# Kernel optimization log

Measured on AMD Instinct MI355X. Metric: run time of the kernel, lower is better.

Reference implementation:

```python
import jax, jax.numpy as jnp
import numpy as np
import math

DIM = 1024

def setup_inputs() -> dict:
    key = jax.random.key(0)
    ks = jax.random.split(key, 5)
    X = jax.random.normal(ks[0], (4, 2048, DIM), dtype=jnp.float32)
    # Linear params (stored as [in, out] so y = x @ W + b)
    W_in = jax.random.normal(ks[1], (DIM, 3 * DIM), dtype=jnp.float32) / math.sqrt(DIM)
    b_in = jnp.zeros((3 * DIM,), dtype=jnp.float32)
    W_out = jax.random.normal(ks[2], (DIM, DIM), dtype=jnp.float32) / math.sqrt(DIM)
    b_out = jnp.zeros((DIM,), dtype=jnp.float32)
    return {"X": X, "W_in": W_in, "b_in": b_in, "W_out": W_out, "b_out": b_out}

def reference(X, W_in, b_in, W_out, b_out):
    dim = X.shape[-1]
    QKV = X @ W_in + b_in                       # [B, S, 3*dim]
    Q, K, V = jnp.split(QKV, 3, axis=-1)        # each [B, S, dim]
    scores = jnp.einsum('bqd,bkd->bqk', Q, K) / math.sqrt(dim)  # [B, S, S]
    attn = jax.nn.softmax(scores, axis=-1)
    out = jnp.einsum('bqk,bkd->bqd', attn, V)   # [B, S, dim]
    return out @ W_out + b_out
```

## Files before the change

### kernel.cpp

```cpp
#include <hip/hip_runtime.h>
#include <hip/hip_bf16.h>
#include <math.h>

typedef __attribute__((ext_vector_type(8))) __bf16 bf16x8;
typedef __attribute__((ext_vector_type(4))) float f32x4;
typedef __attribute__((ext_vector_type(4))) unsigned int u32x4;

#define DIM 1024
#define SEQ 2048
#define BATCH 4
#define ROWS (BATCH*SEQ)

#define BAR() do { asm volatile("" ::: "memory"); __builtin_amdgcn_s_barrier(); asm volatile("" ::: "memory"); } while(0)
#define WAITV(n) asm volatile("s_waitcnt vmcnt(" #n ")" ::: "memory")
#define WAITL(n) asm volatile("s_waitcnt lgkmcnt(" #n ")" ::: "memory")
#define SCHED0() __builtin_amdgcn_sched_barrier(0)
#define PRIO(x) __builtin_amdgcn_s_setprio(x)

#define DSR(d, a, off) do { u32x4 _t; \
  asm volatile("ds_read_b128 %0, %1 offset:" #off : "=v"(_t) : "v"(a)); \
  (d) = __builtin_bit_cast(bf16x8, _t); } while(0)

__device__ __forceinline__ unsigned short f2bf(float f) {
  unsigned int u = __float_as_uint(f);
  u += 0x7FFF + ((u >> 16) & 1);
  return (unsigned short)(u >> 16);
}
__device__ __forceinline__ unsigned short to_bf_bits(float v) { return f2bf(v); }
__device__ __forceinline__ unsigned short to_bf_bits(unsigned short v) { return v; }

__device__ __forceinline__ void gload_lds16(const void* g, void* lds) {
  __builtin_amdgcn_global_load_lds((__attribute__((address_space(1))) void*)g,
                                   (__attribute__((address_space(3))) void*)lds,
                                   16, 0, 0);
}

__global__ __launch_bounds__(256)
void conv_f32_bf16(const float* __restrict__ src, unsigned short* __restrict__ dst, int n8) {
  int i = blockIdx.x * blockDim.x + threadIdx.x;
  if (i >= n8) return;
  const float4* s = reinterpret_cast<const float4*>(src) + (size_t)i * 2;
  float4 a = s[0], b = s[1];
  union { unsigned short h[8]; uint4 v; } p;
  p.h[0]=f2bf(a.x); p.h[1]=f2bf(a.y); p.h[2]=f2bf(a.z); p.h[3]=f2bf(a.w);
  p.h[4]=f2bf(b.x); p.h[5]=f2bf(b.y); p.h[6]=f2bf(b.z); p.h[7]=f2bf(b.w);
  reinterpret_cast<uint4*>(dst)[i] = p.v;
}

template<typename Tin>
__global__ __launch_bounds__(1024)
void transpose_conv(const Tin* __restrict__ src, int ldsrc, size_t sstride,
                    unsigned short* __restrict__ dst, int lddst, size_t dstride) {
  __shared__ unsigned short tile[32][33];
  const Tin* s = src + (size_t)blockIdx.z * sstride;
  unsigned short* d = dst + (size_t)blockIdx.z * dstride;
  int tx = threadIdx.x, ty = threadIdx.y;
  int r = blockIdx.y * 32 + ty, c = blockIdx.x * 32 + tx;
  tile[ty][tx] = to_bf_bits(s[(size_t)r * ldsrc + c]);
  __syncthreads();
  d[(size_t)(blockIdx.x * 32 + ty) * lddst + blockIdx.y * 32 + tx] = tile[tx][ty];
}

#define EPI_QKV 0
#define EPI_F32 1
#define EPI_BF16 2
#define EPI_BIAS_F32 3

template<int BN, int EPI>
__global__ __launch_bounds__(512, 2)
void gemm8(const unsigned short* __restrict__ A, int lda, size_t sA,
           const unsigned short* __restrict__ B, int ldb, size_t sB,
           void* __restrict__ C, int ldc, size_t sC,
           const float* __restrict__ bias, int K) {
  constexpr int NREP = BN / 64;
  constexpr int NW = 16 * NREP;
  __shared__ unsigned short As[2 * 256 * 64];
  __shared__ unsigned short Bs[2 * BN * 64];

  const int tid = threadIdx.x;
  const int lane = tid & 63, wave = tid >> 6;
  const int wm = wave >> 2, wn = wave & 3;
  const int fr = lane & 15, fk = lane >> 4;
  const int tileM = blockIdx.y * 256, tileN = blockIdx.x * BN;
  const unsigned short* Ab = A + (size_t)blockIdx.z * sA;
  const unsigned short* Bb = B + (size_t)blockIdx.z * sB;

  const int srow = tid >> 3;
  const int sg = (tid & 7) ^ (srow & 7);

  auto stageA = [&](int buf, int half, int k0) {
#pragma unroll
    for (int q = 0; q < 2; ++q) {
      int rl = half * 128 + q * 64 + srow;
      gload_lds16(Ab + (size_t)(tileM + rl) * lda + k0 + sg * 8,
                  &As[buf * (256 * 64) + rl * 64 + (tid & 7) * 8]);
    }
  };
  auto stageB = [&](int buf, int half, int k0) {
#pragma unroll
    for (int q = 0; q < 2; ++q) {
      int rl = half * 128 + q * 64 + srow;
      gload_lds16(Bb + (size_t)(tileN + rl) * ldb + k0 + sg * 8,
                  &Bs[buf * (BN * 64) + rl * 64 + (tid & 7) * 8]);
    }
  };

  f32x4 acc[8][NREP];
#pragma unroll
  for (int m = 0; m < 8; ++m)
#pragma unroll
    for (int n = 0; n < NREP; ++n) acc[m][n] = (f32x4){0.f, 0.f, 0.f, 0.f};

  const int NS = K >> 6;
  const unsigned asb = (unsigned)(size_t)(__attribute__((address_space(3))) unsigned short*)As;
  const unsigned bsb = (unsigned)(size_t)(__attribute__((address_space(3))) unsigned short*)Bs;
  const unsigned aoff = (unsigned)((wm * 128 + fr) * 128 + ((fk ^ (fr & 7)) << 4));
  const unsigned boff = (unsigned)((wn * NW + fr) * 128 + ((fk ^ (fr & 7)) << 4));
  auto aBase = [&](int b) { return asb + (unsigned)b * 32768u + aoff; };
  auto bBase = [&](int b) { return bsb + (unsigned)b * (unsigned)(BN * 128) + boff; };

  if constexpr (BN == 256) {
    bf16x8 afLo[4][2], afHi[4][2], bgA[2][2], bgB[2][2];
    stageB(0, 0, 0); stageB(0, 1, 0); stageA(0, 0, 0); stageA(0, 1, 0);
    if (NS > 1) { stageB(1, 0, 64); stageB(1, 1, 64); WAITV(4); } else { WAITV(0); }
    BAR();
    {
      unsigned a0 = aBase(0), a1 = a0 ^ 64u, b0 = bBase(0), b1 = b0 ^ 64u;
      DSR(afLo[0][0], a0, 0); DSR(afLo[1][0], a0, 2048); DSR(afLo[2][0], a0, 4096); DSR(afLo[3][0], a0, 6144);
      DSR(afLo[0][1], a1, 0); DSR(afLo[1][1], a1, 2048); DSR(afLo[2][1], a1, 4096); DSR(afLo[3][1], a1, 6144);
      DSR(bgA[0][0], b0, 0); DSR(bgA[1][0], b0, 2048);
      DSR(bgA[0][1], b1, 0); DSR(bgA[1][1], b1, 2048);
    }
    for (int t = 0; t < NS; ++t) {
      const int cb = t & 1, nb = cb ^ 1;
      const unsigned cA0 = aBase(cb), cA1 = cA0 ^ 64u, cB0 = bBase(cb), cB1 = cB0 ^ 64u;
      const unsigned nA0 = aBase(nb), nA1 = nA0 ^ 64u, nB0 = bBase(nb), nB1 = nB0 ^ 64u;
      const int k1 = (t + 1) << 6, k2 = (t + 2) << 6;
      DSR(bgB[0][0], cB0, 4096); DSR(bgB[1][0], cB0, 6144);
      DSR(bgB[0][1], cB1, 4096); DSR(bgB[1][1], cB1, 6144);
      if (t + 1 < NS) stageA(nb, 0, k1);
      BAR(); WAITL(4); SCHED0();
      PRIO(1);
#pragma unroll
      for (int kk = 0; kk < 2; ++kk)
#pragma unroll
        for (int m = 0; m < 4; ++m)
#pragma unroll
          for (int n = 0; n < 2; ++n)
            acc[m][n] = __builtin_amdgcn_mfma_f32_16x16x32_bf16(afLo[m][kk], bgA[n][kk], acc[m][n], 0, 0, 0);
      PRIO(0); SCHED0();
      BAR();
      DSR(afHi[0][0], cA0, 8192); DSR(afHi[1][0], cA0, 10240); DSR(afHi[2][0], cA0, 12288); DSR(afHi[3][0], cA0, 14336);
      DSR(afHi[0][1], cA1, 8192); DSR(afHi[1][1], cA1, 10240); DSR(afHi[2][1], cA1, 12288); DSR(afHi[3][1], cA1, 14336);
      if (t + 1 < NS) stageA(nb, 1, k1);
      if (t + 2 < NS) stageB(cb, 0, k2);
      BAR(); WAITL(8); SCHED0();
      PRIO(1);
#pragma unroll
      for (int kk = 0; kk < 2; ++kk)
#pragma unroll
        for (int m = 0; m < 4; ++m)
#pragma unroll
          for (int n = 0; n < 2; ++n)
            acc[m][2 + n] = __builtin_amdgcn_mfma_f32_16x16x32_bf16(afLo[m][kk], bgB[n][kk], acc[m][2 + n], 0, 0, 0);
      PRIO(0); SCHED0();
      BAR();
      if (t + 2 < NS) stageB(cb, 1, k2);
      BAR(); WAITL(0); SCHED0();
      PRIO(1);
#pragma unroll
      for (int kk = 0; kk < 2; ++kk)
#pragma unroll
        for (int m = 0; m < 4; ++m)
#pragma unroll
          for (int n = 0; n < 2; ++n)
            acc[4 + m][n] = __builtin_amdgcn_mfma_f32_16x16x32_bf16(afHi[m][kk], bgA[n][kk], acc[4 + m][n], 0, 0, 0);
      PRIO(0); SCHED0();
      if (t + 1 < NS) { if (t + 2 < NS) { WAITV(4); } else { WAITV(0); } }
      BAR();
      if (t + 1 < NS) {
        DSR(afLo[0][0], nA0, 0); DSR(afLo[1][0], nA0, 2048); DSR(afLo[2][0], nA0, 4096); DSR(afLo[3][0], nA0, 6144);
        DSR(afLo[0][1], nA1, 0); DSR(afLo[1][1], nA1, 2048); DSR(afLo[2][1], nA1, 4096); DSR(afLo[3][1], nA1, 6144);
        DSR(bgA[0][0], nB0, 0); DSR(bgA[1][0], nB0, 2048);
        DSR(bgA[0][1], nB1, 0); DSR(bgA[1][1], nB1, 2048);
      }
      SCHED0();
      PRIO(1);
#pragma unroll
      for (int kk = 0; kk < 2; ++kk)
#pragma unroll
        for (int m = 0; m < 4; ++m)
#pragma unroll
          for (int n = 0; n < 2; ++n)
            acc[4 + m][2 + n] = __builtin_amdgcn_mfma_f32_16x16x32_bf16(afHi[m][kk], bgB[n][kk], acc[4 + m][2 + n], 0, 0, 0);
      PRIO(0); SCHED0();
      BAR();
    }
  } else {
    bf16x8 afLo[4][2], afHi[4][2], bgA[2][2];
    stageB(0, 0, 0); stageA(0, 0, 0); stageA(0, 1, 0);
    if (NS > 1) { stageB(1, 0, 64); WAITV(2); } else { WAITV(0); }
    BAR();
    for (int t = 0; t < NS; ++t) {
      const int cb = t & 1, nb = cb ^ 1;
      const unsigned aA0 = aBase(cb), aA1 = aA0 ^ 64u;
      const unsigned bB0 = bBase(cb), bB1 = bB0 ^ 64u;
      const int k1 = (t + 1) << 6, k2 = (t + 2) << 6;
      DSR(afLo[0][0], aA0, 0); DSR(afLo[1][0], aA0, 2048); DSR(afLo[2][0], aA0, 4096); DSR(afLo[3][0], aA0, 6144);
      DSR(bgA[0][0], bB0, 0); DSR(bgA[1][0], bB0, 2048);
      if (t + 1 < NS) stageA(nb, 0, k1);
      BAR(); WAITL(0); SCHED0();
      PRIO(1);
#pragma unroll
      for (int m = 0; m < 4; ++m)
#pragma unroll
        for (int n = 0; n < 2; ++n)
          acc[m][n] = __builtin_amdgcn_mfma_f32_16x16x32_bf16(afLo[m][0], bgA[n][0], acc[m][n], 0, 0, 0);
      PRIO(0); SCHED0();
      BAR();
      DSR(afLo[0][1], aA1, 0); DSR(afLo[1][1], aA1, 2048); DSR(afLo[2][1], aA1, 4096); DSR(afLo[3][1], aA1, 6144);
      DSR(bgA[0][1], bB1, 0); DSR(bgA[1][1], bB1, 2048);
      if (t + 1 < NS) stageA(nb, 1, k1);
      BAR(); WAITL(0); SCHED0();
      PRIO(1);
#pragma unroll
      for (int m = 0; m < 4; ++m)
#pragma unroll
        for (int n = 0; n < 2; ++n)
          acc[m][n] = __builtin_amdgcn_mfma_f32_16x16x32_bf16(afLo[m][1], bgA[n][1], acc[m][n], 0, 0, 0);
      PRIO(0); SCHED0();
      BAR();
      DSR(afHi[0][0], aA0, 8192); DSR(afHi[1][0], aA0, 10240); DSR(afHi[2][0], aA0, 12288); DSR(afHi[3][0], aA0, 14336);
      DSR(afHi[0][1], aA1, 8192); DSR(afHi[1][1], aA1, 10240); DSR(afHi[2][1], aA1, 12288); DSR(afHi[3][1], aA1, 14336);
      if (t + 2 < NS) stageB(cb, 0, k2);
      BAR(); WAITL(0); SCHED0();
      PRIO(1);
#pragma unroll
      for (int m = 0; m < 4; ++m)
#pragma unroll
        for (int n = 0; n < 2; ++n)
          acc[4 + m][n] = __builtin_amdgcn_mfma_f32_16x16x32_bf16(afHi[m][0], bgA[n][0], acc[4 + m][n], 0, 0, 0);
      PRIO(0); SCHED0();
      BAR();
      PRIO(1);
#pragma unroll
      for (int m = 0; m < 4; ++m)
#pragma unroll
        for (int n = 0; n < 2; ++n)
          acc[4 + m][n] = __builtin_amdgcn_mfma_f32_16x16x32_bf16(afHi[m][1], bgA[n][1], acc[4 + m][n], 0, 0, 0);
      PRIO(0); SCHED0();
      if (t + 1 < NS) { if (t + 2 < NS) { WAITV(2); } else { WAITV(0); } }
      BAR();
    }
  }

#pragma unroll
  for (int m = 0; m < 8; ++m)
#pragma unroll
    for (int n = 0; n < NREP; ++n)
#pragma unroll
      for (int j = 0; j < 4; ++j) {
        int row = tileM + wm * 128 + m * 16 + fk * 4 + j;
        int col = tileN + wn * NW + n * 16 + fr;
        float v = acc[m][n][j];
        if (EPI == EPI_QKV) {
          v += bias[col];
          if (col < DIM) v *= 0.03125f;
          ((unsigned short*)C + (size_t)blockIdx.z * sC)[(size_t)row * ldc + col] = f2bf(v);
        } else if (EPI == EPI_BF16) {
          ((unsigned short*)C + (size_t)blockIdx.z * sC)[(size_t)row * ldc + col] = f2bf(v);
        } else if (EPI == EPI_BIAS_F32) {
          ((float*)C + (size_t)blockIdx.z * sC)[(size_t)row * ldc + col] = v + bias[col];
        } else {
          ((float*)C + (size_t)blockIdx.z * sC)[(size_t)row * ldc + col] = v;
        }
      }
}

__global__ __launch_bounds__(256)
void softmax_kernel(float* __restrict__ S, size_t zstride) {
  __shared__ float red[8];
  float* row = S + (size_t)blockIdx.y * zstride + (size_t)blockIdx.x * SEQ;
  const int tid = threadIdx.x;
  const int lane = tid & 63, wave = tid >> 6;
  const float4* src = reinterpret_cast<const float4*>(row) + tid * 2;
  float4 a = src[0], b = src[1];
  float v[8] = {a.x, a.y, a.z, a.w, b.x, b.y, b.z, b.w};
  float m = v[0];
#pragma unroll
  for (int i = 1; i < 8; ++i) m = fmaxf(m, v[i]);
  for (int o = 32; o; o >>= 1) m = fmaxf(m, __shfl_xor(m, o));
  if (lane == 0) red[wave] = m;
  __syncthreads();
  m = fmaxf(fmaxf(red[0], red[1]), fmaxf(red[2], red[3]));
  float e[8], s = 0.f;
#pragma unroll
  for (int i = 0; i < 8; ++i) { e[i] = __expf(v[i] - m); s += e[i]; }
  for (int o = 32; o; o >>= 1) s += __shfl_xor(s, o);
  if (lane == 0) red[4 + wave] = s;
  __syncthreads();
  s = red[4] + red[5] + red[6] + red[7];
  float inv = 1.f / s;
  union { unsigned short h[8]; uint4 u; } p;
#pragma unroll
  for (int i = 0; i < 8; ++i) p.h[i] = f2bf(e[i] * inv);
  reinterpret_cast<uint4*>(row)[tid] = p.u;
}

extern "C" void kernel_launch(void* const* d_in, const int* in_sizes, int n_in,
                              void* d_out, int out_size, void* d_ws, size_t ws_size,
                              hipStream_t stream) {
  const float* X     = (const float*)d_in[0];
  const float* W_in  = (const float*)d_in[1];
  const float* b_in  = (const float*)d_in[2];
  const float* W_out = (const float*)d_in[3];
  const float* b_out = (const float*)d_in[4];
  float* out = (float*)d_out;
  char* ws = (char*)d_ws;

  size_t o = 0;
  auto alloc = [&](size_t bytes) { size_t r = o; o += (bytes + 255) & ~(size_t)255; return r; };
  unsigned short* Xbf   = (unsigned short*)(ws + alloc((size_t)ROWS * DIM * 2));
  unsigned short* WinT  = (unsigned short*)(ws + alloc((size_t)3 * DIM * DIM * 2));
  unsigned short* WoutT = (unsigned short*)(ws + alloc((size_t)DIM * DIM * 2));
  unsigned short* QKV   = (unsigned short*)(ws + alloc((size_t)ROWS * 3 * DIM * 2));
  size_t fixed = o;
  size_t per_batch = (((size_t)SEQ * SEQ * 4 + 255) & ~(size_t)255) +
                     (((size_t)DIM * SEQ * 2 + 255) & ~(size_t)255);
  int G = (ws_size >= fixed + 4 * per_batch) ? BATCH : 1;
  float*          Sc = (float*)(ws + alloc((size_t)G * SEQ * SEQ * 4));
  unsigned short* Vt = (unsigned short*)(ws + alloc((size_t)G * DIM * SEQ * 2));
  unsigned short* Ob = Xbf;

  conv_f32_bf16<<<(ROWS * DIM / 8 + 255) / 256, 256, 0, stream>>>(X, Xbf, ROWS * DIM / 8);
  transpose_conv<float><<<dim3(3 * DIM / 32, DIM / 32, 1), dim3(32, 32), 0, stream>>>(
      W_in, 3 * DIM, 0, WinT, DIM, 0);
  transpose_conv<float><<<dim3(DIM / 32, DIM / 32, 1), dim3(32, 32), 0, stream>>>(
      W_out, DIM, 0, WoutT, DIM, 0);
  gemm8<128, EPI_QKV><<<dim3(3 * DIM / 128, ROWS / 256, 1), 512, 0, stream>>>(
      Xbf, DIM, 0, WinT, DIM, 0, QKV, 3 * DIM, 0, b_in, DIM);

  for (int b0 = 0; b0 < BATCH; b0 += G) {
    const unsigned short* Qb = QKV + (size_t)b0 * SEQ * 3 * DIM;
    const unsigned short* Kb = Qb + DIM;
    const unsigned short* Vb = Qb + 2 * DIM;
    transpose_conv<unsigned short><<<dim3(DIM / 32, SEQ / 32, G), dim3(32, 32), 0, stream>>>(
        Vb, 3 * DIM, (size_t)SEQ * 3 * DIM, Vt, SEQ, (size_t)DIM * SEQ);
    gemm8<256, EPI_F32><<<dim3(SEQ / 256, SEQ / 256, G), 512, 0, stream>>>(
        Qb, 3 * DIM, (size_t)SEQ * 3 * DIM, Kb, 3 * DIM, (size_t)SEQ * 3 * DIM,
        Sc, SEQ, (size_t)SEQ * SEQ, nullptr, DIM);
    softmax_kernel<<<dim3(SEQ, G), 256, 0, stream>>>(Sc, (size_t)SEQ * SEQ);
    gemm8<128, EPI_BF16><<<dim3(DIM / 128, SEQ / 256, G), 512, 0, stream>>>(
        (const unsigned short*)Sc, 2 * SEQ, (size_t)2 * SEQ * SEQ,
        Vt, SEQ, (size_t)DIM * SEQ,
        Ob + (size_t)b0 * SEQ * DIM, DIM, (size_t)SEQ * DIM, nullptr, SEQ);
  }
  gemm8<128, EPI_BIAS_F32><<<dim3(DIM / 128, ROWS / 256, 1), 512, 0, stream>>>(
      Ob, DIM, 0, WoutT, DIM, 0, out, DIM, 0, b_out, DIM);
}
```

Measured before the change: 227.9 us.

## Fuse V transpose into QKV GEMM epilogue and swizzle GEMM block order

The QKV projection epilogue now writes the V columns directly in transposed layout into a dedicated Vt buffer, which removes the separate transpose kernel launch and its read/write pass over V. Separately, all gemm8 instances remap block indices with a stride-8 swizzle, intended to improve L2 locality across workgroups. Vt is now allocated for all batches up front, which increases the fixed workspace and could reduce G in low-memory cases. The transposed stores are 8-byte strided writes, which may coalesce less well than the original row-major stores.

```diff
diff --git a/kernel.cpp b/kernel.cpp
--- a/kernel.cpp
+++ b/kernel.cpp
@@ -71,7 +71,8 @@
 void gemm8(const unsigned short* __restrict__ A, int lda, size_t sA,
            const unsigned short* __restrict__ B, int ldb, size_t sB,
            void* __restrict__ C, int ldc, size_t sC,
-           const float* __restrict__ bias, int K) {
+           const float* __restrict__ bias, int K,
+           unsigned short* __restrict__ VtOut, size_t sVt) {
   constexpr int NREP = BN / 64;
   constexpr int NW = 16 * NREP;
   __shared__ unsigned short As[2 * 256 * 64];
@@ -81,7 +82,15 @@
   const int lane = tid & 63, wave = tid >> 6;
   const int wm = wave >> 2, wn = wave & 3;
   const int fr = lane & 15, fk = lane >> 4;
-  const int tileM = blockIdx.y * 256, tileN = blockIdx.x * BN;
+
+  const int nwg = gridDim.x * gridDim.y;
+  const int flat = blockIdx.x + gridDim.x * blockIdx.y;
+  int bx = blockIdx.x, by = blockIdx.y;
+  if ((nwg & 7) == 0) {
+    int swz = (flat & 7) * (nwg >> 3) + (flat >> 3);
+    bx = swz % gridDim.x; by = swz / gridDim.x;
+  }
+  const int tileM = by * 256, tileN = bx * BN;
   const unsigned short* Ab = A + (size_t)blockIdx.z * sA;
   const unsigned short* Bb = B + (size_t)blockIdx.z * sB;
 
@@ -254,27 +263,45 @@
     }
   }
 
-#pragma unroll
-  for (int m = 0; m < 8; ++m)
-#pragma unroll
-    for (int n = 0; n < NREP; ++n)
-#pragma unroll
-      for (int j = 0; j < 4; ++j) {
-        int row = tileM + wm * 128 + m * 16 + fk * 4 + j;
+  if (EPI == EPI_QKV && tileN >= 2 * DIM) {
+    const int b = tileM >> 11;
+    const int sb0 = (tileM & (SEQ - 1)) + wm * 128;
+    unsigned short* Vb = VtOut + (size_t)b * sVt;
+#pragma unroll
+    for (int m = 0; m < 8; ++m)
+#pragma unroll
+      for (int n = 0; n < NREP; ++n) {
         int col = tileN + wn * NW + n * 16 + fr;
-        float v = acc[m][n][j];
-        if (EPI == EPI_QKV) {
-          v += bias[col];
-          if (col < DIM) v *= 0.03125f;
-          ((unsigned short*)C + (size_t)blockIdx.z * sC)[(size_t)row * ldc + col] = f2bf(v);
-        } else if (EPI == EPI_BF16) {
-          ((unsigned short*)C + (size_t)blockIdx.z * sC)[(size_t)row * ldc + col] = f2bf(v);
-        } else if (EPI == EPI_BIAS_F32) {
-          ((float*)C + (size_t)blockIdx.z * sC)[(size_t)row * ldc + col] = v + bias[col];
-        } else {
-          ((float*)C + (size_t)blockIdx.z * sC)[(size_t)row * ldc + col] = v;
+        int d = col - 2 * DIM;
+        int s = sb0 + m * 16 + fk * 4;
+        union { unsigned short h[4]; uint2 u; } p;
+#pragma unroll
+        for (int j = 0; j < 4; ++j) p.h[j] = f2bf(acc[m][n][j] + bias[col]);
+        *reinterpret_cast<uint2*>(&Vb[(size_t)d * SEQ + s]) = p.u;
+      }
+  } else {
+#pragma unroll
+    for (int m = 0; m < 8; ++m)
+#pragma unroll
+      for (int n = 0; n < NREP; ++n)
+#pragma unroll
+        for (int j = 0; j < 4; ++j) {
+          int row = tileM + wm * 128 + m * 16 + fk * 4 + j;
+          int col = tileN + wn * NW + n * 16 + fr;
+          float v = acc[m][n][j];
+          if (EPI == EPI_QKV) {
+            v += bias[col];
+            if (col < DIM) v *= 0.03125f;
+            ((unsigned short*)C + (size_t)blockIdx.z * sC)[(size_t)row * ldc + col] = f2bf(v);
+          } else if (EPI == EPI_BF16) {
+            ((unsigned short*)C + (size_t)blockIdx.z * sC)[(size_t)row * ldc + col] = f2bf(v);
+          } else if (EPI == EPI_BIAS_F32) {
+            ((float*)C + (size_t)blockIdx.z * sC)[(size_t)row * ldc + col] = v + bias[col];
+          } else {
+            ((float*)C + (size_t)blockIdx.z * sC)[(size_t)row * ldc + col] = v;
+          }
         }
-      }
+  }
 }
 
 __global__ __launch_bounds__(256)
@@ -324,12 +351,11 @@
   unsigned short* WinT  = (unsigned short*)(ws + alloc((size_t)3 * DIM * DIM * 2));
   unsigned short* WoutT = (unsigned short*)(ws + alloc((size_t)DIM * DIM * 2));
   unsigned short* QKV   = (unsigned short*)(ws + alloc((size_t)ROWS * 3 * DIM * 2));
+  unsigned short* Vt    = (unsigned short*)(ws + alloc((size_t)BATCH * DIM * SEQ * 2));
   size_t fixed = o;
-  size_t per_batch = (((size_t)SEQ * SEQ * 4 + 255) & ~(size_t)255) +
-                     (((size_t)DIM * SEQ * 2 + 255) & ~(size_t)255);
+  size_t per_batch = (((size_t)SEQ * SEQ * 4 + 255) & ~(size_t)255);
   int G = (ws_size >= fixed + 4 * per_batch) ? BATCH : 1;
-  float*          Sc = (float*)(ws + alloc((size_t)G * SEQ * SEQ * 4));
-  unsigned short* Vt = (unsigned short*)(ws + alloc((size_t)G * DIM * SEQ * 2));
+  float* Sc = (float*)(ws + alloc((size_t)G * SEQ * SEQ * 4));
   unsigned short* Ob = Xbf;
 
   conv_f32_bf16<<<(ROWS * DIM / 8 + 255) / 256, 256, 0, stream>>>(X, Xbf, ROWS * DIM / 8);
@@ -338,23 +364,21 @@
   transpose_conv<float><<<dim3(DIM / 32, DIM / 32, 1), dim3(32, 32), 0, stream>>>(
       W_out, DIM, 0, WoutT, DIM, 0);
   gemm8<128, EPI_QKV><<<dim3(3 * DIM / 128, ROWS / 256, 1), 512, 0, stream>>>(
-      Xbf, DIM, 0, WinT, DIM, 0, QKV, 3 * DIM, 0, b_in, DIM);
+      Xbf, DIM, 0, WinT, DIM, 0, QKV, 3 * DIM, 0, b_in, DIM,
+      Vt, (size_t)DIM * SEQ);
 
   for (int b0 = 0; b0 < BATCH; b0 += G) {
     const unsigned short* Qb = QKV + (size_t)b0 * SEQ * 3 * DIM;
     const unsigned short* Kb = Qb + DIM;
-    const unsigned short* Vb = Qb + 2 * DIM;
-    transpose_conv<unsigned short><<<dim3(DIM / 32, SEQ / 32, G), dim3(32, 32), 0, stream>>>(
-        Vb, 3 * DIM, (size_t)SEQ * 3 * DIM, Vt, SEQ, (size_t)DIM * SEQ);
     gemm8<256, EPI_F32><<<dim3(SEQ / 256, SEQ / 256, G), 512, 0, stream>>>(
         Qb, 3 * DIM, (size_t)SEQ * 3 * DIM, Kb, 3 * DIM, (size_t)SEQ * 3 * DIM,
-        Sc, SEQ, (size_t)SEQ * SEQ, nullptr, DIM);
+        Sc, SEQ, (size_t)SEQ * SEQ, nullptr, DIM, nullptr, 0);
     softmax_kernel<<<dim3(SEQ, G), 256, 0, stream>>>(Sc, (size_t)SEQ * SEQ);
     gemm8<128, EPI_BF16><<<dim3(DIM / 128, SEQ / 256, G), 512, 0, stream>>>(
         (const unsigned short*)Sc, 2 * SEQ, (size_t)2 * SEQ * SEQ,
-        Vt, SEQ, (size_t)DIM * SEQ,
-        Ob + (size_t)b0 * SEQ * DIM, DIM, (size_t)SEQ * DIM, nullptr, SEQ);
+        Vt + (size_t)b0 * DIM * SEQ, SEQ, (size_t)DIM * SEQ,
+        Ob + (size_t)b0 * SEQ * DIM, DIM, (size_t)SEQ * DIM, nullptr, SEQ, nullptr, 0);
   }
   gemm8<128, EPI_BIAS_F32><<<dim3(DIM / 128, ROWS / 256, 1), 512, 0, stream>>>(
-      Ob, DIM, 0, WoutT, DIM, 0, out, DIM, 0, b_out, DIM);
-}
+      Ob, DIM, 0, WoutT, DIM, 0, out, DIM, 0, b_out, DIM, nullptr, 0);
+}
```

Result: faster. 211.0 us (-7.4%).
